# Performance work log

Measured on AMD Instinct MI355X. Metric: run time of the kernel, lower is better.

The kernel has to match this reference:

```python
import jax, jax.numpy as jnp
from jax import lax
import numpy as np

# Geometry derived from module.calibrate() for input [2,64,768,768], k=3, s=1, bcount=(16,16)
N, CIN, COUT, H, W = 2, 64, 64, 768, 768
K, STRIDE = 3, 1
BC = 16            # block count per spatial dim
PAD = 1            # total pad 2 -> 1 each side (H and W)
BSIZE = 50         # gathered block size (input space, padded input is 770)
BOUT = 48          # conv output size per block
BSTR = 48          # block stride (= bsize - k + stride); also scatter stride
NBLK = 256
BN_EPS = 1e-3


def setup_inputs() -> dict:
    key = jax.random.key(0)
    ks = jax.random.split(key, 7)
    x = jax.random.normal(ks[0], (N, CIN, H, W), jnp.float32)
    conv_w = jax.random.normal(ks[1], (COUT, CIN, K, K), jnp.float32) * 0.05
    conv_b = jax.random.normal(ks[2], (COUT,), jnp.float32) * 0.1
    gamma = jax.random.uniform(ks[3], (COUT,), jnp.float32, 0.5, 1.5)
    beta = jax.random.normal(ks[4], (COUT,), jnp.float32) * 0.1
    run_mean = jax.random.normal(ks[5], (COUT,), jnp.float32) * 0.1
    run_var = jax.random.uniform(ks[6], (COUT,), jnp.float32, 0.5, 1.5)
    # unique active blocks (n, bh, bw) as in ReduceMask.active_block_indices
    rng = np.random.default_rng(0)
    all_blocks = np.stack(np.meshgrid(np.arange(N), np.arange(BC), np.arange(BC),
                                      indexing='ij'), axis=-1).reshape(-1, 3)
    sel = rng.permutation(all_blocks.shape[0])[:NBLK]
    abi = jnp.asarray(all_blocks[sel], jnp.int32)
    return dict(x=x, conv_w=conv_w, conv_b=conv_b, gamma=gamma, beta=beta,
                run_mean=run_mean, run_var=run_var, active_block_indices=abi)


def reference(x, conv_w, conv_b, gamma, beta, run_mean, run_var, active_block_indices):
    # pad as in F.pad(padding_params)
    xp = jnp.pad(x, ((0, 0), (0, 0), (PAD, PAD), (PAD, PAD)))  # [N,C,770,770]
    nidx = active_block_indices[:, 0]                          # [B]
    hh = active_block_indices[:, 1][:, None] * BSTR + jnp.arange(BSIZE)[None, :]  # [B,50]
    ww = active_block_indices[:, 2][:, None] * BSTR + jnp.arange(BSIZE)[None, :]  # [B,50]
    # sparse_gather: extract [B,50,50,C] blocks (vectorized advanced indexing)
    xp_nhwc = xp.transpose(0, 2, 3, 1)
    p = xp_nhwc[nidx[:, None, None], hh[:, :, None], ww[:, None, :]]   # [B,50,50,C]
    p = p.transpose(0, 3, 1, 2)                                        # [B,C,50,50]
    # conv2d (VALID) + bias
    q = lax.conv_general_dilated(p, conv_w, (STRIDE, STRIDE), 'VALID')
    q = q + conv_b[None, :, None, None]                                # [B,COUT,48,48]
    # BatchNorm (inference: running stats) + ReLU
    inv = gamma / jnp.sqrt(run_var + BN_EPS)
    q = q * inv[None, :, None, None] + (beta - run_mean * inv)[None, :, None, None]
    q = jax.nn.relu(q)
    # sparse_scatter (add=False) into [N,COUT,768,768]; blocks are non-overlapping
    ho = active_block_indices[:, 1][:, None] * BSTR + jnp.arange(BOUT)[None, :]
    wo = active_block_indices[:, 2][:, None] * BSTR + jnp.arange(BOUT)[None, :]
    y = jnp.zeros((N, H, W, COUT), x.dtype)
    y = y.at[nidx[:, None, None], ho[:, :, None], wo[:, None, :]].set(q.transpose(0, 2, 3, 1))
    return y.transpose(0, 3, 1, 2)
```

## Files before the change

### kernel.cpp

```cpp
#include <hip/hip_runtime.h>


typedef __attribute__((ext_vector_type(8))) short short8;
typedef __attribute__((ext_vector_type(4))) float floatx4;

#define WS_SCALE 0
#define WS_SHIFT 64
#define WS_FLAGS 128
#define WS_WA    640

#define CONV_WGS 1536
#define ZERO_WGS 4096

__device__ __forceinline__ short f2bf(float f) {
  unsigned u = __builtin_bit_cast(unsigned, f);
  u += 0x7fffu + ((u >> 16) & 1u);
  return (short)(u >> 16);
}

__global__ __launch_bounds__(256) void prep_kernel(
    const float* __restrict__ conv_w,
    const float* __restrict__ conv_b,
    const float* __restrict__ gamma,
    const float* __restrict__ beta,
    const float* __restrict__ run_mean,
    const float* __restrict__ run_var,
    const int* __restrict__ abi,
    float* __restrict__ ws) {
  int tid = threadIdx.x;
  if (blockIdx.x == 0) {
    int* flags = (int*)(ws + WS_FLAGS);
    flags[tid] = 0;
    flags[tid + 256] = 0;
    __syncthreads();
    int n = abi[3 * tid + 0];
    int bh = abi[3 * tid + 1];
    int bw = abi[3 * tid + 2];
    flags[n * 256 + bh * 16 + bw] = 1;
    if (tid < 64) {
      float inv = gamma[tid] * rsqrtf(run_var[tid] + 1e-3f);
      ws[WS_SCALE + tid] = inv;
      ws[WS_SHIFT + tid] = (conv_b[tid] - run_mean[tid]) * inv + beta[tid];
    }
  }
  short* wa = (short*)(ws + WS_WA);
  for (int d = blockIdx.x * 256 + tid; d < 49152; d += 64 * 256) {
    int j = d & 7;
    int q = (d >> 3) & 3;
    int cout = (d >> 5) & 63;
    int ks = d >> 11;
    int kt = ks % 3;
    int cc = ks / 3;
    int tap = kt * 4 + q;
    short v = 0;
    if (tap < 9) {
      int ci = cc * 8 + j;
      int dy = tap / 3;
      int dx = tap - dy * 3;
      v = f2bf(conv_w[((cout * 64 + ci) * 3 + dy) * 3 + dx]);
    }
    wa[d] = v;
  }
}

__global__ __launch_bounds__(512, 4) void main_kernel(
    const float* __restrict__ x,
    const float* __restrict__ ws_f,
    const int* __restrict__ abi,
    float* __restrict__ out) {
  __shared__ __align__(16) short lds[2][4008];
  int b = blockIdx.x;
  int tid = threadIdx.x;

  if (b >= CONV_WGS) {
    const int* flags = (const int*)(ws_f + WS_FLAGS);
    int z = b - CONV_WGS;
    int tile = z >> 3;
    int part = z & 7;
    if (flags[tile]) return;
    int n = tile >> 8;
    int bh = (tile >> 4) & 15;
    int bw = tile & 15;
    float* base = out + (((n * 64 + part * 8) * 768 + bh * 48)) * 768 + bw * 48;
    float4 zv = make_float4(0.f, 0.f, 0.f, 0.f);
#pragma unroll
    for (int i = 0; i < 9; ++i) {
      int idx = i * 512 + tid;
      int f = idx % 12;
      int t2 = idx / 12;
      int rr = t2 % 48;
      int c = t2 / 48;
      *((float4*)(base + (c * 768 + rr) * (size_t)768) + f) = zv;
    }
    return;
  }

  int blk = b / 6;
  int strip = b - blk * 6;
  int n = abi[3 * blk + 0];
  int bh = abi[3 * blk + 1];
  int bw = abi[3 * blk + 2];
  int h0 = bh * 48 + strip * 8;
  int w0 = bw * 48;

  int lane = tid & 63;
  int wv = tid >> 6;
  int ln15 = lane & 15;
  int quad = lane >> 4;

  const float* xn = x + (size_t)n * 64 * 768 * 768;
  const short* wa = (const short*)(ws_f + WS_WA);

  if (tid < 8) { lds[0][4000 + tid] = 0; lds[1][4000 + tid] = 0; }

  int bA[3][3];
#pragma unroll
  for (int kt = 0; kt < 3; ++kt) {
    int tap = kt * 4 + quad;
    if (tap < 9) {
      int dy = tap / 3;
      int dx = tap - dy * 3;
      int a0 = ((wv + dy) * 50 + ln15 + dx) * 16;
#pragma unroll
      for (int c16 = 0; c16 < 3; ++c16) bA[kt][c16] = a0 + c16 * 256;
    } else {
#pragma unroll
      for (int c16 = 0; c16 < 3; ++c16) bA[kt][c16] = 8000;
    }
  }

  auto load_chunk = [&](int cc8, float4* pf) {
#pragma unroll
    for (int i = 0; i < 3; ++i) {
      int e = i * 512 + tid;
      float4 v = make_float4(0.f, 0.f, 0.f, 0.f);
      if (e < 1120) {
        int f = e % 14;
        int t = e / 14;
        int r = t % 10;
        int ci = t / 10;
        int gh = h0 - 1 + r;
        int gw0 = w0 - 4 + 4 * f;
        if ((unsigned)gh < 768u) {
          const float* rp = xn + ((size_t)(cc8 + ci) * 768 + gh) * 768;
          if (gw0 >= 0 && gw0 <= 764) {
            v = *(const float4*)(rp + gw0);
          } else {
#pragma unroll
            for (int j = 0; j < 4; ++j) {
              int gw = gw0 + j;
              if ((unsigned)gw < 768u) ((float*)&v)[j] = rp[gw];
            }
          }
        }
      }
      pf[i] = v;
    }
  };
  auto store_chunk = [&](int bsel, const float4* pf) {
#pragma unroll
    for (int i = 0; i < 3; ++i) {
      int e = i * 512 + tid;
      if (e < 1120) {
        int f = e % 14;
        int t = e / 14;
        int r = t % 10;
        int ci = t / 10;
        const float* vp = (const float*)&pf[i];
#pragma unroll
        for (int j = 0; j < 4; ++j) {
          int c = 4 * f - 3 + j;
          if ((unsigned)c < 50u)
            lds[bsel][(r * 50 + c) * 8 + ci] = f2bf(vp[j]);
        }
      }
    }
  };

  float4 pf[3];
  load_chunk(0, pf);
  store_chunk(0, pf);
  __syncthreads();

  floatx4 acc[3][4];
#pragma unroll
  for (int c16 = 0; c16 < 3; ++c16)
#pragma unroll
    for (int mt = 0; mt < 4; ++mt)
      acc[c16][mt] = (floatx4){0.f, 0.f, 0.f, 0.f};

  for (int cc = 0; cc < 8; ++cc) {
    int bsel = cc & 1;
    if (cc < 7) load_chunk((cc + 1) * 8, pf);
    const char* lbase = (const char*)lds[bsel];
#pragma unroll
    for (int kt = 0; kt < 3; ++kt) {
      int ks = cc * 3 + kt;
      short8 af[4];
#pragma unroll
      for (int mt = 0; mt < 4; ++mt)
        af[mt] = *(const short8*)(wa + ks * 2048 + (mt * 16 + ln15) * 32 + quad * 8);
#pragma unroll
      for (int c16 = 0; c16 < 3; ++c16) {
        short8 bf = *(const short8*)(lbase + bA[kt][c16]);
#pragma unroll
        for (int mt = 0; mt < 4; ++mt)
          acc[c16][mt] = __builtin_amdgcn_mfma_f32_16x16x32_bf16(
              af[mt], bf, acc[c16][mt], 0, 0, 0);
      }
    }
    if (cc < 7) store_chunk(bsel ^ 1, pf);
    __syncthreads();
  }

  const float* scale = ws_f + WS_SCALE;
  const float* shift = ws_f + WS_SHIFT;
  float* outn = out + (size_t)n * 64 * 768 * 768;
  int gr = h0 + wv;
#pragma unroll
  for (int mt = 0; mt < 4; ++mt) {
#pragma unroll
    for (int reg = 0; reg < 4; ++reg) {
      int cout = mt * 16 + quad * 4 + reg;
      float sc = scale[cout];
      float sh = shift[cout];
#pragma unroll
      for (int c16 = 0; c16 < 3; ++c16) {
        float vv = fmaf(acc[c16][mt][reg], sc, sh);
        vv = vv > 0.f ? vv : 0.f;
        outn[((size_t)cout * 768 + gr) * 768 + w0 + c16 * 16 + ln15] = vv;
      }
    }
  }
}

extern "C" void kernel_launch(void* const* d_in, const int* in_sizes, int n_in,
                              void* d_out, int out_size, void* d_ws, size_t ws_size,
                              hipStream_t stream) {
  const float* x = (const float*)d_in[0];
  const float* conv_w = (const float*)d_in[1];
  const float* conv_b = (const float*)d_in[2];
  const float* gamma = (const float*)d_in[3];
  const float* beta = (const float*)d_in[4];
  const float* run_mean = (const float*)d_in[5];
  const float* run_var = (const float*)d_in[6];
  const int* abi = (const int*)d_in[7];
  float* out = (float*)d_out;
  float* ws = (float*)d_ws;

  prep_kernel<<<64, 256, 0, stream>>>(conv_w, conv_b, gamma, beta,
                                      run_mean, run_var, abi, ws);
  main_kernel<<<CONV_WGS + ZERO_WGS, 512, 0, stream>>>(x, ws, abi, out);
}
```

Before: 582.1 us.

## Stage input tiles via global_load_lds DMA and pad bf16 LDS layout

```diff
diff --git a/kernel.cpp b/kernel.cpp
--- a/kernel.cpp
+++ b/kernel.cpp
@@ -16,6 +16,12 @@
   unsigned u = __builtin_bit_cast(unsigned, f);
   u += 0x7fffu + ((u >> 16) & 1u);
   return (short)(u >> 16);
+}
+
+__device__ __forceinline__ void gload_lds16(const float* g, float* l) {
+  __builtin_amdgcn_global_load_lds(
+      (const __attribute__((address_space(1))) void*)g,
+      (__attribute__((address_space(3))) void*)l, 16, 0, 0);
 }
 
 __global__ __launch_bounds__(256) void prep_kernel(
@@ -63,12 +69,14 @@
   }
 }
 
-__global__ __launch_bounds__(512, 4) void main_kernel(
+__global__ __launch_bounds__(512, 8) void main_kernel(
     const float* __restrict__ x,
     const float* __restrict__ ws_f,
     const int* __restrict__ abi,
     float* __restrict__ out) {
-  __shared__ __align__(16) short lds[2][4008];
+  __shared__ __align__(16) float Fs[4608];
+  __shared__ __align__(16) short bfb[2][4864];
+
   int b = blockIdx.x;
   int tid = threadIdx.x;
 
@@ -110,77 +118,68 @@
 
   const float* xn = x + (size_t)n * 64 * 768 * 768;
   const short* wa = (const short*)(ws_f + WS_WA);
-
-  if (tid < 8) { lds[0][4000 + tid] = 0; lds[1][4000 + tid] = 0; }
-
-  int bA[3][3];
+  const short* wap = wa + ln15 * 32 + quad * 8;
+
+  if (tid < 8) {
+    bfb[0][4560 + tid] = 0; bfb[0][4704 + tid] = 0; bfb[0][4848 + tid] = 0;
+    bfb[1][4560 + tid] = 0; bfb[1][4704 + tid] = 0; bfb[1][4848 + tid] = 0;
+  }
+
+  int bA[3];
 #pragma unroll
   for (int kt = 0; kt < 3; ++kt) {
     int tap = kt * 4 + quad;
     if (tap < 9) {
       int dy = tap / 3;
       int dx = tap - dy * 3;
-      int a0 = ((wv + dy) * 50 + ln15 + dx) * 16;
-#pragma unroll
-      for (int c16 = 0; c16 < 3; ++c16) bA[kt][c16] = a0 + c16 * 256;
+      int cx = ln15 + dx;
+      bA[kt] = ((wv + dy) * 57 + cx + (cx >> 3)) * 16;
     } else {
-#pragma unroll
-      for (int c16 = 0; c16 < 3; ++c16) bA[kt][c16] = 8000;
-    }
-  }
-
-  auto load_chunk = [&](int cc8, float4* pf) {
+      bA[kt] = 9120;
+    }
+  }
+
+  auto dma_slot = [&](int c, int s) {
+    int ci = s / 140;
+    int rem = s - ci * 140;
+    int r = rem / 14;
+    int f = rem - r * 14;
+    int gh = h0 - 1 + r;
+    int gw0 = w0 - 4 + 4 * f;
+    const float* src = xn;
+    if (s < 1120 && (unsigned)gh < 768u && (unsigned)gw0 <= 764u)
+      src = xn + (size_t)c * (8 * 768 * 768) + ((size_t)ci * 768 + gh) * 768 + gw0;
+    gload_lds16(src, &Fs[s * 4]);
+  };
+  auto dma_chunk = [&](int c) {
+    dma_slot(c, tid);
+    dma_slot(c, 512 + tid);
+    if (wv < 2) dma_slot(c, 1024 + tid);
+  };
+
+  auto convert = [&](int bsel) {
 #pragma unroll
     for (int i = 0; i < 3; ++i) {
-      int e = i * 512 + tid;
-      float4 v = make_float4(0.f, 0.f, 0.f, 0.f);
-      if (e < 1120) {
-        int f = e % 14;
-        int t = e / 14;
-        int r = t % 10;
-        int ci = t / 10;
-        int gh = h0 - 1 + r;
-        int gw0 = w0 - 4 + 4 * f;
-        if ((unsigned)gh < 768u) {
-          const float* rp = xn + ((size_t)(cc8 + ci) * 768 + gh) * 768;
-          if (gw0 >= 0 && gw0 <= 764) {
-            v = *(const float4*)(rp + gw0);
-          } else {
-#pragma unroll
-            for (int j = 0; j < 4; ++j) {
-              int gw = gw0 + j;
-              if ((unsigned)gw < 768u) ((float*)&v)[j] = rp[gw];
-            }
-          }
+      int s = i * 512 + tid;
+      if (i == 2 && s >= 1120) break;
+      int ci = s / 140;
+      int rem = s - ci * 140;
+      int r = rem / 14;
+      int f = rem - r * 14;
+      bool ok = ((unsigned)(h0 - 1 + r) < 768u) && ((unsigned)(w0 - 4 + 4 * f) <= 764u);
+      float4 v = *(const float4*)&Fs[s * 4];
+      int cb = 4 * f - 3;
+      int rb = r * 57;
+#pragma unroll
+      for (int j = 0; j < 4; ++j) {
+        int cth = cb + j;
+        if ((unsigned)cth < 50u) {
+          int u = rb + cth + (cth >> 3);
+          bfb[bsel][u * 8 + ci] = ok ? f2bf(((const float*)&v)[j]) : (short)0;
         }
       }
-      pf[i] = v;
     }
   };
-  auto store_chunk = [&](int bsel, const float4* pf) {
-#pragma unroll
-    for (int i = 0; i < 3; ++i) {
-      int e = i * 512 + tid;
-      if (e < 1120) {
-        int f = e % 14;
-        int t = e / 14;
-        int r = t % 10;
-        int ci = t / 10;
-        const float* vp = (const float*)&pf[i];
-#pragma unroll
-        for (int j = 0; j < 4; ++j) {
-          int c = 4 * f - 3 + j;
-          if ((unsigned)c < 50u)
-            lds[bsel][(r * 50 + c) * 8 + ci] = f2bf(vp[j]);
-        }
-      }
-    }
-  };
-
-  float4 pf[3];
-  load_chunk(0, pf);
-  store_chunk(0, pf);
-  __syncthreads();
 
   floatx4 acc[3][4];
 #pragma unroll
@@ -189,34 +188,41 @@
     for (int mt = 0; mt < 4; ++mt)
       acc[c16][mt] = (floatx4){0.f, 0.f, 0.f, 0.f};
 
+  dma_chunk(0);
+  __syncthreads();
+  convert(0);
+  __syncthreads();
+
   for (int cc = 0; cc < 8; ++cc) {
     int bsel = cc & 1;
-    if (cc < 7) load_chunk((cc + 1) * 8, pf);
-    const char* lbase = (const char*)lds[bsel];
+    if (cc < 7) dma_chunk(cc + 1);
+    const char* lb = (const char*)bfb[bsel];
 #pragma unroll
     for (int kt = 0; kt < 3; ++kt) {
       int ks = cc * 3 + kt;
       short8 af[4];
 #pragma unroll
       for (int mt = 0; mt < 4; ++mt)
-        af[mt] = *(const short8*)(wa + ks * 2048 + (mt * 16 + ln15) * 32 + quad * 8);
+        af[mt] = *(const short8*)(wap + ks * 2048 + mt * 512);
 #pragma unroll
       for (int c16 = 0; c16 < 3; ++c16) {
-        short8 bf = *(const short8*)(lbase + bA[kt][c16]);
+        short8 bf = *(const short8*)(lb + bA[kt] + c16 * 288);
 #pragma unroll
         for (int mt = 0; mt < 4; ++mt)
           acc[c16][mt] = __builtin_amdgcn_mfma_f32_16x16x32_bf16(
               af[mt], bf, acc[c16][mt], 0, 0, 0);
       }
     }
-    if (cc < 7) store_chunk(bsel ^ 1, pf);
     __syncthreads();
+    if (cc < 7) {
+      convert(bsel ^ 1);
+      __syncthreads();
+    }
   }
 
   const float* scale = ws_f + WS_SCALE;
   const float* shift = ws_f + WS_SHIFT;
-  float* outn = out + (size_t)n * 64 * 768 * 768;
-  int gr = h0 + wv;
+  float* op = out + (size_t)n * 64 * 768 * 768 + (size_t)(h0 + wv) * 768 + (w0 + ln15);
 #pragma unroll
   for (int mt = 0; mt < 4; ++mt) {
 #pragma unroll
@@ -228,7 +234,7 @@
       for (int c16 = 0; c16 < 3; ++c16) {
         float vv = fmaf(acc[c16][mt][reg], sc, sh);
         vv = vv > 0.f ? vv : 0.f;
-        outn[((size_t)cout * 768 + gr) * 768 + w0 + c16 * 16 + ln15] = vv;
+        op[(size_t)cout * 589824 + c16 * 16] = vv;
       }
     }
   }
```

Measured after the change: 1.037 ms. 1.78x slower.

## Interleave conv and zero-fill workgroups and pad LDS rows to avoid bank conflicts

Applied to the files above, without the earlier changes.

```diff
diff --git a/kernel.cpp b/kernel.cpp
--- a/kernel.cpp
+++ b/kernel.cpp
@@ -11,6 +11,7 @@
 
 #define CONV_WGS 1536
 #define ZERO_WGS 4096
+#define TOTAL_WGS (CONV_WGS + ZERO_WGS)
 
 __device__ __forceinline__ short f2bf(float f) {
   unsigned u = __builtin_bit_cast(unsigned, f);
@@ -68,13 +69,18 @@
     const float* __restrict__ ws_f,
     const int* __restrict__ abi,
     float* __restrict__ out) {
-  __shared__ __align__(16) short lds[2][4008];
-  int b = blockIdx.x;
+  __shared__ __align__(16) short lds[2][4864];
+
+  int braw = blockIdx.x;
   int tid = threadIdx.x;
 
-  if (b >= CONV_WGS) {
+  int before = (int)(((long long)braw * CONV_WGS) / TOTAL_WGS);
+  int after  = (int)(((long long)(braw + 1) * CONV_WGS) / TOTAL_WGS);
+  bool is_conv = after > before;
+
+  if (!is_conv) {
     const int* flags = (const int*)(ws_f + WS_FLAGS);
-    int z = b - CONV_WGS;
+    int z = braw - before;
     int tile = z >> 3;
     int part = z & 7;
     if (flags[tile]) return;
@@ -95,6 +101,7 @@
     return;
   }
 
+  int b = before;
   int blk = b / 6;
   int strip = b - blk * 6;
   int n = abi[3 * blk + 0];
@@ -110,22 +117,24 @@
 
   const float* xn = x + (size_t)n * 64 * 768 * 768;
   const short* wa = (const short*)(ws_f + WS_WA);
-
-  if (tid < 8) { lds[0][4000 + tid] = 0; lds[1][4000 + tid] = 0; }
-
-  int bA[3][3];
+  const short* wap = wa + ln15 * 32 + quad * 8;
+
+  if (tid < 8) {
+    lds[0][4560 + tid] = 0; lds[0][4704 + tid] = 0; lds[0][4848 + tid] = 0;
+    lds[1][4560 + tid] = 0; lds[1][4704 + tid] = 0; lds[1][4848 + tid] = 0;
+  }
+
+  int bA[3];
 #pragma unroll
   for (int kt = 0; kt < 3; ++kt) {
     int tap = kt * 4 + quad;
     if (tap < 9) {
       int dy = tap / 3;
       int dx = tap - dy * 3;
-      int a0 = ((wv + dy) * 50 + ln15 + dx) * 16;
-#pragma unroll
-      for (int c16 = 0; c16 < 3; ++c16) bA[kt][c16] = a0 + c16 * 256;
+      int cx = ln15 + dx;
+      bA[kt] = ((wv + dy) * 57 + cx + (cx >> 3)) * 16;
     } else {
-#pragma unroll
-      for (int c16 = 0; c16 < 3; ++c16) bA[kt][c16] = 8000;
+      bA[kt] = 9120;
     }
   }
 
@@ -170,8 +179,10 @@
 #pragma unroll
         for (int j = 0; j < 4; ++j) {
           int c = 4 * f - 3 + j;
-          if ((unsigned)c < 50u)
-            lds[bsel][(r * 50 + c) * 8 + ci] = f2bf(vp[j]);
+          if ((unsigned)c < 50u) {
+            int u = r * 57 + c + (c >> 3);
+            lds[bsel][u * 8 + ci] = f2bf(vp[j]);
+          }
         }
       }
     }
@@ -192,17 +203,17 @@
   for (int cc = 0; cc < 8; ++cc) {
     int bsel = cc & 1;
     if (cc < 7) load_chunk((cc + 1) * 8, pf);
-    const char* lbase = (const char*)lds[bsel];
+    const char* lb = (const char*)lds[bsel];
 #pragma unroll
     for (int kt = 0; kt < 3; ++kt) {
       int ks = cc * 3 + kt;
       short8 af[4];
 #pragma unroll
       for (int mt = 0; mt < 4; ++mt)
-        af[mt] = *(const short8*)(wa + ks * 2048 + (mt * 16 + ln15) * 32 + quad * 8);
+        af[mt] = *(const short8*)(wap + ks * 2048 + mt * 512);
 #pragma unroll
       for (int c16 = 0; c16 < 3; ++c16) {
-        short8 bf = *(const short8*)(lbase + bA[kt][c16]);
+        short8 bf = *(const short8*)(lb + bA[kt] + c16 * 288);
 #pragma unroll
         for (int mt = 0; mt < 4; ++mt)
           acc[c16][mt] = __builtin_amdgcn_mfma_f32_16x16x32_bf16(
@@ -215,8 +226,7 @@
 
   const float* scale = ws_f + WS_SCALE;
   const float* shift = ws_f + WS_SHIFT;
-  float* outn = out + (size_t)n * 64 * 768 * 768;
-  int gr = h0 + wv;
+  float* op = out + (size_t)n * 64 * 768 * 768 + (size_t)(h0 + wv) * 768 + (w0 + ln15);
 #pragma unroll
   for (int mt = 0; mt < 4; ++mt) {
 #pragma unroll
@@ -228,7 +238,7 @@
       for (int c16 = 0; c16 < 3; ++c16) {
         float vv = fmaf(acc[c16][mt][reg], sc, sh);
         vv = vv > 0.f ? vv : 0.f;
-        outn[((size_t)cout * 768 + gr) * 768 + w0 + c16 * 16 + ln15] = vv;
+        op[(size_t)cout * 589824 + c16 * 16] = vv;
       }
     }
   }
@@ -250,5 +260,5 @@
 
   prep_kernel<<<64, 256, 0, stream>>>(conv_w, conv_b, gamma, beta,
                                       run_mean, run_var, abi, ws);
-  main_kernel<<<CONV_WGS + ZERO_WGS, 512, 0, stream>>>(x, ws, abi, out);
-}
+  main_kernel<<<TOTAL_WGS, 512, 0, stream>>>(x, ws, abi, out);
+}
```

Measured after the change: 617.1 us. +6.0%, slower.
